# Kernel optimization log

Hardware: AMD Instinct MI355X
Metric: run time of the kernel (lower is better)

The kernel has to match this reference:

```python
import jax, jax.numpy as jnp
import numpy as np

EPS = 1e-6
CLASS_LAMBDA = 1.0
BBOX_LAMBDA = 1.0
IOU_LAMBDA = 1.0

B, Q, C1, T = 8, 900, 92, 1600  # batch, queries, num_classes+1, total targets


def _make_boxes(u):
    # turn uniform [.,4] noise into valid xyxy boxes in [0,1]
    xy = u[..., :2] * 0.7
    wh = u[..., 2:] * 0.3 + 0.01
    return jnp.concatenate([xy, xy + wh], axis=-1)


def setup_inputs() -> dict:
    key = jax.random.key(0)
    k1, k2, k3, k4 = jax.random.split(key, 4)
    pred_logits = jax.random.normal(k1, (B, Q, C1), dtype=jnp.float32)
    pred_bbox = _make_boxes(jax.random.uniform(k2, (B, Q, 4), dtype=jnp.float32))
    tgt_ids = jax.random.randint(k3, (T,), 0, 91, dtype=jnp.int32)
    tgt_bbox = _make_boxes(jax.random.uniform(k4, (T, 4), dtype=jnp.float32))
    return {"pred_logits": pred_logits, "pred_bbox": pred_bbox,
            "tgt_ids": tgt_ids, "tgt_bbox": tgt_bbox}


def _ciou_pairwise(b1, b2):
    # b1: [M,4], b2: [N,4] xyxy -> CIoU [M,N]
    b1 = b1[:, None, :]
    b2 = b2[None, :, :]
    x1 = jnp.maximum(b1[..., 0], b2[..., 0])
    y1 = jnp.maximum(b1[..., 1], b2[..., 1])
    x2 = jnp.minimum(b1[..., 2], b2[..., 2])
    y2 = jnp.minimum(b1[..., 3], b2[..., 3])
    inter = jnp.clip(x2 - x1, 0.0) * jnp.clip(y2 - y1, 0.0)
    w1 = b1[..., 2] - b1[..., 0]
    h1 = b1[..., 3] - b1[..., 1]
    w2 = b2[..., 2] - b2[..., 0]
    h2 = b2[..., 3] - b2[..., 1]
    union = w1 * h1 + w2 * h2 - inter
    iou = inter / (union + EPS)
    cw = jnp.maximum(b1[..., 2], b2[..., 2]) - jnp.minimum(b1[..., 0], b2[..., 0])
    ch = jnp.maximum(b1[..., 3], b2[..., 3]) - jnp.minimum(b1[..., 1], b2[..., 1])
    convex_diag_sq = cw ** 2 + ch ** 2
    center_dist_sq = ((b2[..., 0] + b2[..., 2] - b1[..., 0] - b1[..., 2]) ** 2
                      + (b2[..., 1] + b2[..., 3] - b1[..., 1] - b1[..., 3]) ** 2)
    dist_penalty = center_dist_sq / (convex_diag_sq + EPS) / 4.0
    v = (4.0 / jnp.pi ** 2) * (jnp.arctan(w2 / (h2 + EPS)) - jnp.arctan(w1 / (h1 + EPS))) ** 2
    alpha = jax.lax.stop_gradient(v / (1.0 + EPS - iou + v))  # torch no_grad
    return iou - dist_penalty - alpha * v


def reference(pred_logits, pred_bbox, tgt_ids, tgt_bbox):
    bsz, nq = pred_logits.shape[:2]
    out_prob = jax.nn.softmax(pred_logits.reshape(bsz * nq, -1), axis=-1)  # [BQ, C+1]
    out_bbox = pred_bbox.reshape(bsz * nq, 4)                              # [BQ, 4]
    cost_class = -out_prob[:, tgt_ids]                                     # [BQ, T]
    # L1 cdist
    cost_bbox = jnp.sum(jnp.abs(out_bbox[:, None, :] - tgt_bbox[None, :, :]), axis=-1)
    cost_iou = -_ciou_pairwise(out_bbox, tgt_bbox)                         # [BQ, T]
    cost = BBOX_LAMBDA * cost_bbox + CLASS_LAMBDA * cost_class + IOU_LAMBDA * cost_iou
    return cost.reshape(bsz, nq, -1)  # [B, Q, T]
```

## Files before the change

### kernel.cpp

```cpp
#include <hip/hip_runtime.h>
#include <math.h>

#define EPSF 1e-6f

constexpr int B_ = 8, Q_ = 900, C1_ = 92, T_ = 1600;
constexpr int NROW = B_ * Q_;
constexpr int PSTRIDE = 96;
constexpr int RPB = 16;
constexpr int TPB = 320;

__global__ __launch_bounds__(64) void precompute_kernel(
    const float* __restrict__ logits,
    const float* __restrict__ pbox,
    const float* __restrict__ tbox,
    float* __restrict__ probs,
    float* __restrict__ predd,
    float* __restrict__ tgtd)
{
    const int bid  = blockIdx.x;
    const int lane = threadIdx.x;

    if (bid < NROW) {
        const float* lrow = logits + (size_t)bid * C1_;
        float x0 = -INFINITY, x1 = -INFINITY;
        if (lane < C1_)      x0 = lrow[lane];
        if (lane + 64 < C1_) x1 = lrow[lane + 64];
        float m = fmaxf(x0, x1);
        #pragma unroll
        for (int off = 32; off; off >>= 1) m = fmaxf(m, __shfl_xor(m, off));
        float e0 = (lane < C1_)      ? __expf(x0 - m) : 0.0f;
        float e1 = (lane + 64 < C1_) ? __expf(x1 - m) : 0.0f;
        float s = e0 + e1;
        #pragma unroll
        for (int off = 32; off; off >>= 1) s += __shfl_xor(s, off);
        const float inv = 1.0f / s;
        float* prow = probs + (size_t)bid * PSTRIDE;
        if (lane < C1_)      prow[lane]      = e0 * inv;
        if (lane + 64 < C1_) prow[lane + 64] = e1 * inv;

        if (lane == 0) {
            const float bx1 = pbox[bid * 4 + 0];
            const float by1 = pbox[bid * 4 + 1];
            const float bx2 = pbox[bid * 4 + 2];
            const float by2 = pbox[bid * 4 + 3];
            const float w = bx2 - bx1, h = by2 - by1;
            float* d = predd + bid * 8;
            d[0] = bx1; d[1] = by1; d[2] = bx2; d[3] = by2;
            d[4] = w * h;
            d[5] = atanf(w / (h + EPSF));
            d[6] = bx1 + bx2;
            d[7] = by1 + by2;
        }
    } else {
        const int t = (bid - NROW) * 64 + lane;
        if (t < T_) {
            const float bx1 = tbox[t * 4 + 0];
            const float by1 = tbox[t * 4 + 1];
            const float bx2 = tbox[t * 4 + 2];
            const float by2 = tbox[t * 4 + 3];
            const float w = bx2 - bx1, h = by2 - by1;
            float* d = tgtd + t * 8;
            d[0] = bx1; d[1] = by1; d[2] = bx2; d[3] = by2;
            d[4] = w * h;
            d[5] = atanf(w / (h + EPSF));
            d[6] = bx1 + bx2;
            d[7] = by1 + by2;
        }
    }
}

__global__ __launch_bounds__(TPB) void cost_kernel(
    const float* __restrict__ probs,
    const float* __restrict__ predd,
    const float* __restrict__ tgtd,
    const int*   __restrict__ ids,
    float* __restrict__ out)
{
    __shared__ float sprobs[RPB * PSTRIDE];
    __shared__ float spredd[RPB * 8];

    const int tid  = threadIdx.x;
    const int t    = blockIdx.x * TPB + tid;
    const int row0 = blockIdx.y * RPB;

    {
        const float4* gp4 = (const float4*)(probs + (size_t)row0 * PSTRIDE);
        float4* sp4 = (float4*)sprobs;
        sp4[tid] = gp4[tid];
        if (tid < RPB * PSTRIDE / 4 - TPB)
            sp4[tid + TPB] = gp4[tid + TPB];
        const float4* gd4 = (const float4*)(predd + (size_t)row0 * 8);
        float4* sd4 = (float4*)spredd;
        if (tid < RPB * 8 / 4)
            sd4[tid] = gd4[tid];
    }

    const float4 ta = *(const float4*)(tgtd + (size_t)t * 8);
    const float4 tb = *(const float4*)(tgtd + (size_t)t * 8 + 4);
    const int id = ids[t];
    const float tx1 = ta.x, ty1 = ta.y, tx2 = ta.z, ty2 = ta.w;
    const float area2 = tb.x, atan2t = tb.y, sx2 = tb.z, sy2 = tb.w;

    __syncthreads();

    float* outp = out + (size_t)row0 * T_ + t;
    #pragma unroll 4
    for (int r = 0; r < RPB; ++r) {
        const float4 pa = *(const float4*)(spredd + r * 8);
        const float4 pb = *(const float4*)(spredd + r * 8 + 4);
        const float px1 = pa.x, py1 = pa.y, px2 = pa.z, py2 = pa.w;
        const float area1 = pb.x, atan1t = pb.y, sx1 = pb.z, sy1 = pb.w;

        const float prob = sprobs[r * PSTRIDE + id];

        const float ix1 = fmaxf(px1, tx1);
        const float iy1 = fmaxf(py1, ty1);
        const float ix2 = fminf(px2, tx2);
        const float iy2 = fminf(py2, ty2);
        const float inter = fmaxf(ix2 - ix1, 0.0f) * fmaxf(iy2 - iy1, 0.0f);
        const float uni = area1 + area2 - inter;
        const float iou = inter * __builtin_amdgcn_rcpf(uni + EPSF);

        const float cw = fmaxf(px2, tx2) - fminf(px1, tx1);
        const float ch = fmaxf(py2, ty2) - fminf(py1, ty1);
        const float diag = cw * cw + ch * ch;
        const float dx = sx2 - sx1, dy = sy2 - sy1;
        const float cdist = dx * dx + dy * dy;
        const float dist_pen = cdist * __builtin_amdgcn_rcpf(diag + EPSF) * 0.25f;

        const float dat = atan2t - atan1t;
        const float v = (4.0f / (float)(M_PI * M_PI)) * dat * dat;
        const float av = v * v * __builtin_amdgcn_rcpf(1.0f + EPSF - iou + v);

        const float ciou = iou - dist_pen - av;

        const float cost_bbox = fabsf(px1 - tx1) + fabsf(py1 - ty1) +
                                fabsf(px2 - tx2) + fabsf(py2 - ty2);

        __builtin_nontemporal_store(cost_bbox - prob - ciou, outp);
        outp += T_;
    }
}

extern "C" void kernel_launch(void* const* d_in, const int* in_sizes, int n_in,
                              void* d_out, int out_size, void* d_ws, size_t ws_size,
                              hipStream_t stream) {
    const float* logits = (const float*)d_in[0];
    const float* pbox   = (const float*)d_in[1];
    const int*   ids    = (const int*)d_in[2];
    const float* tbox   = (const float*)d_in[3];
    float* out = (float*)d_out;

    float* ws    = (float*)d_ws;
    float* probs = ws;
    float* predd = probs + (size_t)NROW * PSTRIDE;
    float* tgtd  = predd + (size_t)NROW * 8;

    const int nTgtBlocks = (T_ + 63) / 64;
    precompute_kernel<<<NROW + nTgtBlocks, 64, 0, stream>>>(
        logits, pbox, tbox, probs, predd, tgtd);

    cost_kernel<<<dim3(T_ / TPB, NROW / RPB), TPB, 0, stream>>>(
        probs, predd, tgtd, ids, out);
}
```

Baseline: 94.47 us.

## Fuse softmax and box precompute into the cost kernel

```diff
diff --git a/kernel.cpp b/kernel.cpp
--- a/kernel.cpp
+++ b/kernel.cpp
@@ -5,113 +5,100 @@
 
 constexpr int B_ = 8, Q_ = 900, C1_ = 92, T_ = 1600;
 constexpr int NROW = B_ * Q_;
-constexpr int PSTRIDE = 96;
 constexpr int RPB = 16;
 constexpr int TPB = 320;
+constexpr int LG = RPB * C1_;
 
-__global__ __launch_bounds__(64) void precompute_kernel(
+__global__ __launch_bounds__(TPB) void fused_cost_kernel(
     const float* __restrict__ logits,
     const float* __restrict__ pbox,
+    const int*   __restrict__ ids,
     const float* __restrict__ tbox,
-    float* __restrict__ probs,
-    float* __restrict__ predd,
-    float* __restrict__ tgtd)
-{
-    const int bid  = blockIdx.x;
-    const int lane = threadIdx.x;
-
-    if (bid < NROW) {
-        const float* lrow = logits + (size_t)bid * C1_;
-        float x0 = -INFINITY, x1 = -INFINITY;
-        if (lane < C1_)      x0 = lrow[lane];
-        if (lane + 64 < C1_) x1 = lrow[lane + 64];
-        float m = fmaxf(x0, x1);
-        #pragma unroll
-        for (int off = 32; off; off >>= 1) m = fmaxf(m, __shfl_xor(m, off));
-        float e0 = (lane < C1_)      ? __expf(x0 - m) : 0.0f;
-        float e1 = (lane + 64 < C1_) ? __expf(x1 - m) : 0.0f;
-        float s = e0 + e1;
-        #pragma unroll
-        for (int off = 32; off; off >>= 1) s += __shfl_xor(s, off);
-        const float inv = 1.0f / s;
-        float* prow = probs + (size_t)bid * PSTRIDE;
-        if (lane < C1_)      prow[lane]      = e0 * inv;
-        if (lane + 64 < C1_) prow[lane + 64] = e1 * inv;
-
-        if (lane == 0) {
-            const float bx1 = pbox[bid * 4 + 0];
-            const float by1 = pbox[bid * 4 + 1];
-            const float bx2 = pbox[bid * 4 + 2];
-            const float by2 = pbox[bid * 4 + 3];
-            const float w = bx2 - bx1, h = by2 - by1;
-            float* d = predd + bid * 8;
-            d[0] = bx1; d[1] = by1; d[2] = bx2; d[3] = by2;
-            d[4] = w * h;
-            d[5] = atanf(w / (h + EPSF));
-            d[6] = bx1 + bx2;
-            d[7] = by1 + by2;
-        }
-    } else {
-        const int t = (bid - NROW) * 64 + lane;
-        if (t < T_) {
-            const float bx1 = tbox[t * 4 + 0];
-            const float by1 = tbox[t * 4 + 1];
-            const float bx2 = tbox[t * 4 + 2];
-            const float by2 = tbox[t * 4 + 3];
-            const float w = bx2 - bx1, h = by2 - by1;
-            float* d = tgtd + t * 8;
-            d[0] = bx1; d[1] = by1; d[2] = bx2; d[3] = by2;
-            d[4] = w * h;
-            d[5] = atanf(w / (h + EPSF));
-            d[6] = bx1 + bx2;
-            d[7] = by1 + by2;
-        }
-    }
-}
-
-__global__ __launch_bounds__(TPB) void cost_kernel(
-    const float* __restrict__ probs,
-    const float* __restrict__ predd,
-    const float* __restrict__ tgtd,
-    const int*   __restrict__ ids,
     float* __restrict__ out)
 {
-    __shared__ float sprobs[RPB * PSTRIDE];
-    __shared__ float spredd[RPB * 8];
+    __shared__ float slog[LG];
+    __shared__ float spred[RPB * 8];
+    __shared__ float sred[RPB * 20];
+    __shared__ float smax[RPB];
+    __shared__ float sinv[RPB];
 
     const int tid  = threadIdx.x;
     const int t    = blockIdx.x * TPB + tid;
     const int row0 = blockIdx.y * RPB;
 
     {
-        const float4* gp4 = (const float4*)(probs + (size_t)row0 * PSTRIDE);
-        float4* sp4 = (float4*)sprobs;
-        sp4[tid] = gp4[tid];
-        if (tid < RPB * PSTRIDE / 4 - TPB)
-            sp4[tid + TPB] = gp4[tid + TPB];
-        const float4* gd4 = (const float4*)(predd + (size_t)row0 * 8);
-        float4* sd4 = (float4*)spredd;
-        if (tid < RPB * 8 / 4)
-            sd4[tid] = gd4[tid];
+        const float4* g4 = (const float4*)(logits + (size_t)row0 * C1_);
+        float4* s4 = (float4*)slog;
+        s4[tid] = g4[tid];
+        if (tid < LG / 4 - TPB)
+            s4[tid + TPB] = g4[tid + TPB];
     }
 
-    const float4 ta = *(const float4*)(tgtd + (size_t)t * 8);
-    const float4 tb = *(const float4*)(tgtd + (size_t)t * 8 + 4);
+    const float4 tb4 = *(const float4*)(tbox + (size_t)t * 4);
     const int id = ids[t];
-    const float tx1 = ta.x, ty1 = ta.y, tx2 = ta.z, ty2 = ta.w;
-    const float area2 = tb.x, atan2t = tb.y, sx2 = tb.z, sy2 = tb.w;
+    const float tx1 = tb4.x, ty1 = tb4.y, tx2 = tb4.z, ty2 = tb4.w;
+    const float w2 = tx2 - tx1, h2 = ty2 - ty1;
+    const float area2  = w2 * h2;
+    const float atan2t = atanf(w2 / (h2 + EPSF));
+    const float sx2 = tx1 + tx2, sy2 = ty1 + ty2;
 
+    if (tid < RPB) {
+        const float4 p = *(const float4*)(pbox + (size_t)(row0 + tid) * 4);
+        const float w = p.z - p.x, h = p.w - p.y;
+        float* d = spred + tid * 8;
+        d[0] = p.x; d[1] = p.y; d[2] = p.z; d[3] = p.w;
+        d[4] = w * h;
+        d[5] = atanf(w / (h + EPSF));
+        d[6] = p.x + p.z;
+        d[7] = p.y + p.w;
+    }
+
+    __syncthreads();
+
+    const int r = tid / 20;
+    const int j = tid - r * 20;
+    {
+        float m = -INFINITY;
+        for (int e = j; e < C1_; e += 20) m = fmaxf(m, slog[r * C1_ + e]);
+        sred[r * 20 + j] = m;
+    }
+    __syncthreads();
+    if (j == 0) {
+        float mm = sred[r * 20];
+        #pragma unroll
+        for (int k = 1; k < 20; ++k) mm = fmaxf(mm, sred[r * 20 + k]);
+        smax[r] = mm;
+    }
+    __syncthreads();
+    {
+        const float mm = smax[r];
+        float s = 0.0f;
+        for (int e = j; e < C1_; e += 20) s += __expf(slog[r * C1_ + e] - mm);
+        sred[r * 20 + j] = s;
+    }
+    __syncthreads();
+    if (j == 0) {
+        float ss = 0.0f;
+        #pragma unroll
+        for (int k = 0; k < 20; ++k) ss += sred[r * 20 + k];
+        sinv[r] = 1.0f / ss;
+    }
+    __syncthreads();
+    for (int i = tid; i < LG; i += TPB) {
+        const int rr = i / C1_;
+        slog[i] = __expf(slog[i] - smax[rr]) * sinv[rr];
+    }
     __syncthreads();
 
     float* outp = out + (size_t)row0 * T_ + t;
     #pragma unroll 4
-    for (int r = 0; r < RPB; ++r) {
-        const float4 pa = *(const float4*)(spredd + r * 8);
-        const float4 pb = *(const float4*)(spredd + r * 8 + 4);
+    for (int rr = 0; rr < RPB; ++rr) {
+        const float4 pa = *(const float4*)(spred + rr * 8);
+        const float4 pb = *(const float4*)(spred + rr * 8 + 4);
         const float px1 = pa.x, py1 = pa.y, px2 = pa.z, py2 = pa.w;
         const float area1 = pb.x, atan1t = pb.y, sx1 = pb.z, sy1 = pb.w;
 
-        const float prob = sprobs[r * PSTRIDE + id];
+        const float prob = slog[rr * C1_ + id];
 
         const float ix1 = fmaxf(px1, tx1);
         const float iy1 = fmaxf(py1, ty1);
@@ -151,15 +138,6 @@
     const float* tbox   = (const float*)d_in[3];
     float* out = (float*)d_out;
 
-    float* ws    = (float*)d_ws;
-    float* probs = ws;
-    float* predd = probs + (size_t)NROW * PSTRIDE;
-    float* tgtd  = predd + (size_t)NROW * 8;
-
-    const int nTgtBlocks = (T_ + 63) / 64;
-    precompute_kernel<<<NROW + nTgtBlocks, 64, 0, stream>>>(
-        logits, pbox, tbox, probs, predd, tgtd);
-
-    cost_kernel<<<dim3(T_ / TPB, NROW / RPB), TPB, 0, stream>>>(
-        probs, predd, tgtd, ids, out);
+    fused_cost_kernel<<<dim3(T_ / TPB, NROW / RPB), TPB, 0, stream>>>(
+        logits, pbox, ids, tbox, out);
 }
```

After: 96.99 us. +2.7%, slower.
